# Performance work log

Measured on AMD Instinct MI355X. Metric: run time of the kernel, lower is better.

## Reference

```python
import jax, jax.numpy as jnp
import numpy as np


def _conv1d_block(x, W, b):
    # reflection pad 1 each side, conv1d k=3 stride=2, relu
    x = jnp.pad(x, ((0, 0), (0, 0), (1, 1)), mode='reflect')
    y = jax.lax.conv_general_dilated(x, W, window_strides=(2,), padding='VALID',
                                     dimension_numbers=('NCH', 'OIH', 'NCH'))
    return jax.nn.relu(y + b[None, :, None])


def setup_inputs() -> dict:
    key = jax.random.key(0)
    ks = jax.random.split(key, 8)
    C, H, E, P = 62, 256, 1024, 32768
    inp = {
        'image_x': jax.random.normal(ks[0], (C, H, H), dtype=jnp.float32),
        'corners': jax.random.uniform(ks[1], (E, 2), dtype=jnp.float32),
        'W0': jax.random.normal(ks[2], (64, C + 2, 3), dtype=jnp.float32) * 0.02,
        'b0': jnp.zeros((64,), jnp.float32),
        'W1': jax.random.normal(ks[3], (64, 64, 3), dtype=jnp.float32) * 0.02,
        'b1': jnp.zeros((64,), jnp.float32),
        'W2': jax.random.normal(ks[4], (64, 64, 3), dtype=jnp.float32) * 0.02,
        'b2': jnp.zeros((64,), jnp.float32),
        'Wf': jax.random.normal(ks[5], (64, 64), dtype=jnp.float32) * 0.05,
        'bf': jnp.zeros((64,), jnp.float32),
        'Wp': jax.random.normal(ks[6], (1, 64), dtype=jnp.float32) * 0.05,
        'bp': jnp.zeros((1,), jnp.float32),
        'num_points': P,  # static stand-in for the host-synced data-dependent count
    }
    return inp


def reference(image_x, corners, W0, b0, W1, b1, W2, b2, Wf, bf, Wp, bp, num_points):
    # edges: [E,4] = (start_xy, end_xy) with wraparound
    edges = jnp.concatenate([corners, jnp.roll(corners, -1, axis=0)], axis=-1)
    starts, ends = edges[:, :2], edges[:, 2:4]
    dirs = ends - starts                                  # [E,2]
    lengths = jnp.linalg.norm(dirs, axis=-1)              # [E]
    length_sum = lengths.sum()
    # arc-length sample offsets (num_points is static)
    offsets = jnp.arange(num_points, dtype=jnp.float32) * (length_sum / num_points)  # [P]
    el2 = jnp.cumsum(lengths)                             # [E]
    el1 = jnp.concatenate([jnp.zeros((1,), lengths.dtype), el2[:-1]])
    # per-(point, edge) interpolation parameter and bin mask
    t = (offsets[:, None] - el1[None, :]) / jnp.maximum(lengths, 1e-4)[None, :]      # [P,E]
    mask = ((offsets[:, None] >= el1[None, :]) & (offsets[:, None] < el2[None, :])).astype(jnp.float32)
    # masked reduction: sum_e mask*(start + t*dir)  (same math, no [P,E,2] temp)
    points = jnp.einsum('pe,ec->pc', mask, starts) + jnp.einsum('pe,ec->pc', mask * t, dirs)  # [P,2]
    H = image_x.shape[1]
    pr = jnp.clip(jnp.round(points * H).astype(jnp.int32), 0, H - 1)  # [P,2]
    x = image_x[:, pr[:, 0], pr[:, 1]]                    # [C,P] fancy gather
    x = jnp.concatenate([x, points.T], axis=0)[None]      # [1,C+2,P]
    x = _conv1d_block(x, W0, b0)
    x = _conv1d_block(x, W1, b1)
    x = _conv1d_block(x, W2, b2)
    x = x.max(axis=-1)                                    # [1,64]
    feat = jax.nn.relu(x @ Wf.T + bf)                     # [1,64]
    pred = jax.nn.sigmoid(feat @ Wp.T + bp).reshape(-1)   # [1]
    return feat, pred
```

## Files before the change

### kernel.cpp

```cpp
#include <hip/hip_runtime.h>
#include <hip/hip_bf16.h>
#include <math.h>

#define EDGES   32768
#define NPTS    32768
#define IMGH    256
#define L0      32768
#define L1      16384
#define L2      8192
#define L3      4096
#define S0      (L1 + 64)
#define B2      31
#define NBC     133

__global__ __launch_bounds__(512) void prep_k(const float* __restrict__ corners,
                                              const float* __restrict__ W0,
                                              const float* __restrict__ W1,
                                              const float* __restrict__ W2,
                                              const float* __restrict__ img,
                                              double* __restrict__ el2loc,
                                              double* __restrict__ partial,
                                              float*  __restrict__ Wt,
                                              float*  __restrict__ imgT)
{
    __shared__ union { double sc[512]; float tile[62][129]; } sm;
    int b = blockIdx.x, t = threadIdx.x;
    if (b < 64) {
        int e  = (b << 9) + t;
        int en = (e + 1) & (EDGES - 1);
        double dx = (double)corners[2*en]   - (double)corners[2*e];
        double dy = (double)corners[2*en+1] - (double)corners[2*e+1];
        sm.sc[t] = sqrt(dx*dx + dy*dy);
        __syncthreads();
        for (int o = 1; o < 512; o <<= 1) {
            double v = (t >= o) ? sm.sc[t - o] : 0.0;
            __syncthreads();
            sm.sc[t] += v;
            __syncthreads();
        }
        el2loc[e] = sm.sc[t];
        if (t == 511) partial[b] = sm.sc[511];
    } else if (b < 136) {
        int idx = ((b - 64) << 9) + t;
        int l   = idx / 12288;
        int rem = idx - l * 12288;
        int row = rem >> 6, o = rem & 63;
        int i   = row / 3,  k = row - i * 3;
        const float* W = (l == 0) ? W0 : ((l == 1) ? W1 : W2);
        Wt[idx] = W[o*192 + i*3 + k];
    } else {
        int pix0 = (b - 136) << 7;
        for (int idx = t; idx < 62*128; idx += 512) {
            int c = idx >> 7, p = idx & 127;
            sm.tile[c][p] = img[c * (IMGH*IMGH) + pix0 + p];
        }
        __syncthreads();
        for (int idx = t; idx < 128*64; idx += 512) {
            int p = idx >> 6, c = idx & 63;
            imgT[(size_t)(pix0 + p) * 64 + c] = (c < 62) ? sm.tile[c][p] : 0.f;
        }
    }
}

__device__ __forceinline__ void stage_ws(float ws[96][64],
                                         const float* __restrict__ Wsrc,
                                         int tid)
{
    const float4* src = (const float4*)Wsrc;
    float4 rw[6];
#pragma unroll
    for (int k = 0; k < 6; ++k) rw[k] = src[k * 256 + tid];
    float4* dst = (float4*)&ws[0][0];
#pragma unroll
    for (int k = 0; k < 6; ++k) dst[k * 256 + tid] = rw[k];
}

__device__ __forceinline__ void conv_half(float acc[16],
                                          const float xs[64][130],
                                          const float ws[96][64],
                                          int ibase, int jl2, int o0)
{
#pragma unroll 4
    for (int ii = 0; ii < 32; ++ii) {
        int i = ibase + ii;
        float x0 = xs[i][jl2], x1 = xs[i][jl2 + 1], x2 = xs[i][jl2 + 2];
        const float4* w0 = (const float4*)&ws[ii*3 + 0][o0];
        const float4* w1 = (const float4*)&ws[ii*3 + 1][o0];
        const float4* w2 = (const float4*)&ws[ii*3 + 2][o0];
#pragma unroll
        for (int q = 0; q < 4; ++q) {
            float4 a = w0[q], b = w1[q], c = w2[q];
            acc[q*4+0] = fmaf(a.x, x0, fmaf(b.x, x1, fmaf(c.x, x2, acc[q*4+0])));
            acc[q*4+1] = fmaf(a.y, x0, fmaf(b.y, x1, fmaf(c.y, x2, acc[q*4+1])));
            acc[q*4+2] = fmaf(a.z, x0, fmaf(b.z, x1, fmaf(c.z, x2, acc[q*4+2])));
            acc[q*4+3] = fmaf(a.w, x0, fmaf(b.w, x1, fmaf(c.w, x2, acc[q*4+3])));
        }
    }
}

__global__ __launch_bounds__(256) void convA_k(const float* __restrict__ corners,
                                               const double* __restrict__ el2loc,
                                               const double* __restrict__ partial,
                                               const float* __restrict__ imgT,
                                               const float* __restrict__ Wt,
                                               const float* __restrict__ bias,
                                               float* __restrict__ Y0)
{
    __shared__ float  xs[64][130];
    __shared__ float  ws[96][64];
    __shared__ double sb[64];
    int tid = threadIdx.x;
    int j0  = blockIdx.x << 6;
    int in0 = (j0 << 1) - 1;

    if (tid < 64) sb[tid] = partial[tid];
    __syncthreads();
#pragma unroll
    for (int o = 1; o < 64; o <<= 1) {
        double v = 0.0;
        if (tid < 64 && tid >= o) v = sb[tid - o];
        __syncthreads();
        if (tid < 64) sb[tid] += v;
        __syncthreads();
    }

    stage_ws(ws, Wt, tid);

    if (tid < 130) {
        int g = in0 + tid;
        if (g < 0)   g = 1;
        if (g >= L0) g = 2*L0 - 2 - g;
        double S   = sb[63];
        double off = (double)g * (S * (1.0 / (double)NPTS));
        int clo = 0, chi = 63;
        while (clo < chi) {
            int cm = (clo + chi) >> 1;
            if (sb[cm] > off) chi = cm; else clo = cm + 1;
        }
        double base = (clo == 0) ? 0.0 : sb[clo - 1];
        int lo = clo << 9, hi = lo + 511;
        while (lo < hi) {
            int mid = (lo + hi) >> 1;
            if (el2loc[mid] + base > off) hi = mid; else lo = mid + 1;
        }
        int e = lo;
        double e1 = (e == 0) ? 0.0
                  : el2loc[e-1] + (((e-1) >= 512) ? sb[((e-1) >> 9) - 1] : 0.0);
        float sxf = corners[2*e], syf = corners[2*e+1];
        int en = (e + 1) & (EDGES - 1);
        double dx = (double)corners[2*en]   - (double)sxf;
        double dy = (double)corners[2*en+1] - (double)syf;
        double len = sqrt(dx*dx + dy*dy);
        double t  = (off - e1) / fmax(len, 0.0001);
        double px = (double)sxf + t * dx;
        double py = (double)syf + t * dy;
        int r0 = (int)rint(px * (double)IMGH); r0 = r0 < 0 ? 0 : (r0 > IMGH-1 ? IMGH-1 : r0);
        int r1 = (int)rint(py * (double)IMGH); r1 = r1 < 0 ? 0 : (r1 > IMGH-1 ? IMGH-1 : r1);
        const float*  row  = imgT + (size_t)((r0 << 8) | r1) * 64;
        const float4* row4 = (const float4*)row;
        float4 rv[15];
#pragma unroll
        for (int c4 = 0; c4 < 15; ++c4) rv[c4] = row4[c4];
        float c60 = row[60], c61 = row[61];
#pragma unroll
        for (int c4 = 0; c4 < 15; ++c4) {
            xs[c4*4 + 0][tid] = rv[c4].x;
            xs[c4*4 + 1][tid] = rv[c4].y;
            xs[c4*4 + 2][tid] = rv[c4].z;
            xs[c4*4 + 3][tid] = rv[c4].w;
        }
        xs[60][tid] = c60;
        xs[61][tid] = c61;
        xs[62][tid] = (float)px;
        xs[63][tid] = (float)py;
    }
    __syncthreads();

    int lane = tid & 63;
    int o0   = (tid >> 6) << 4;
    float acc[16];
#pragma unroll
    for (int m = 0; m < 16; ++m) acc[m] = bias[o0 + m];
    int jl2 = lane << 1;

    conv_half(acc, xs, ws, 0, jl2, o0);
    __syncthreads();
    stage_ws(ws, Wt + 96*64, tid);
    __syncthreads();
    conv_half(acc, xs, ws, 32, jl2, o0);

    int j = j0 + lane;
#pragma unroll
    for (int m = 0; m < 16; ++m)
        Y0[(o0 + m) * S0 + j] = fmaxf(acc[m], 0.f);
}

__global__ __launch_bounds__(256) void convBC_k(const float* __restrict__ Y0,
                                                const float* __restrict__ Wt1,
                                                const float* __restrict__ b1,
                                                const float* __restrict__ Wt2,
                                                const float* __restrict__ b2,
                                                float* __restrict__ pmax)
{
    __shared__ float xs0[32][132];
    __shared__ float t1[64][63];
    __shared__ float ws[96][64];
    int tid = threadIdx.x;
    int b   = blockIdx.x;
    int gbase = 124*b - 3;

    int s  = tid & 63;
    int o0 = (tid >> 6) << 4;
    int j1 = 62*b - 1 + s;
    int jr = (j1 < 0) ? -j1 : (j1 > L2-1 ? L2-1 : j1);
    int col0 = 2*jr - 124*b + 2;

    {
        float r[16];
#pragma unroll
        for (int k = 0; k < 16; ++k) {
            int idx = k*256 + tid;
            int c   = idx >> 7;
            int col = idx & 127;
            int g   = gbase + col;
            if (g < 0)   g = -g;
            if (g >= L1) g = 2*L1 - 2 - g;
            r[k] = Y0[c * S0 + g];
        }
        stage_ws(ws, Wt1, tid);
#pragma unroll
        for (int k = 0; k < 16; ++k) {
            int idx = k*256 + tid;
            xs0[idx >> 7][idx & 127] = r[k];
        }
    }
    __syncthreads();

    float acc1[16];
#pragma unroll
    for (int m = 0; m < 16; ++m) acc1[m] = b1[o0 + m];

#pragma unroll 4
    for (int ii = 0; ii < 32; ++ii) {
        float x0 = xs0[ii][col0], x1 = xs0[ii][col0+1], x2 = xs0[ii][col0+2];
        const float4* w0 = (const float4*)&ws[ii*3 + 0][o0];
        const float4* w1 = (const float4*)&ws[ii*3 + 1][o0];
        const float4* w2 = (const float4*)&ws[ii*3 + 2][o0];
#pragma unroll
        for (int q = 0; q < 4; ++q) {
            float4 a = w0[q], bb = w1[q], c = w2[q];
            acc1[q*4+0] = fmaf(a.x, x0, fmaf(bb.x, x1, fmaf(c.x, x2, acc1[q*4+0])));
            acc1[q*4+1] = fmaf(a.y, x0, fmaf(bb.y, x1, fmaf(c.y, x2, acc1[q*4+1])));
            acc1[q*4+2] = fmaf(a.z, x0, fmaf(bb.z, x1, fmaf(c.z, x2, acc1[q*4+2])));
            acc1[q*4+3] = fmaf(a.w, x0, fmaf(bb.w, x1, fmaf(c.w, x2, acc1[q*4+3])));
        }
    }
    __syncthreads();

    {
        float r[16];
#pragma unroll
        for (int k = 0; k < 16; ++k) {
            int idx = k*256 + tid;
            int c   = idx >> 7;
            int col = idx & 127;
            int g   = gbase + col;
            if (g < 0)   g = -g;
            if (g >= L1) g = 2*L1 - 2 - g;
            r[k] = Y0[(32 + c) * S0 + g];
        }
        stage_ws(ws, Wt1 + 96*64, tid);
#pragma unroll
        for (int k = 0; k < 16; ++k) {
            int idx = k*256 + tid;
            xs0[idx >> 7][idx & 127] = r[k];
        }
    }
    __syncthreads();

#pragma unroll 4
    for (int ii = 0; ii < 32; ++ii) {
        float x0 = xs0[ii][col0], x1 = xs0[ii][col0+1], x2 = xs0[ii][col0+2];
        const float4* w0 = (const float4*)&ws[ii*3 + 0][o0];
        const float4* w1 = (const float4*)&ws[ii*3 + 1][o0];
        const float4* w2 = (const float4*)&ws[ii*3 + 2][o0];
#pragma unroll
        for (int q = 0; q < 4; ++q) {
            float4 a = w0[q], bb = w1[q], c = w2[q];
            acc1[q*4+0] = fmaf(a.x, x0, fmaf(bb.x, x1, fmaf(c.x, x2, acc1[q*4+0])));
            acc1[q*4+1] = fmaf(a.y, x0, fmaf(bb.y, x1, fmaf(c.y, x2, acc1[q*4+1])));
            acc1[q*4+2] = fmaf(a.z, x0, fmaf(bb.z, x1, fmaf(c.z, x2, acc1[q*4+2])));
            acc1[q*4+3] = fmaf(a.w, x0, fmaf(bb.w, x1, fmaf(c.w, x2, acc1[q*4+3])));
        }
    }
    __syncthreads();

    if (s < 63) {
#pragma unroll
        for (int m = 0; m < 16; ++m) t1[o0 + m][s] = fmaxf(acc1[m], 0.f);
    }
    __syncthreads();

    int p  = tid & 31;
    int oc = (tid >> 5) << 3;
    float acc2[8];
#pragma unroll
    for (int q = 0; q < 8; ++q) acc2[q] = b2[oc + q];

    stage_ws(ws, Wt2, tid);
    __syncthreads();
#pragma unroll 4
    for (int ii = 0; ii < 32; ++ii) {
        float x0 = t1[ii][2*p + 0], x1 = t1[ii][2*p + 1], x2 = t1[ii][2*p + 2];
        const float4* w0 = (const float4*)&ws[ii*3 + 0][oc];
        const float4* w1 = (const float4*)&ws[ii*3 + 1][oc];
        const float4* w2 = (const float4*)&ws[ii*3 + 2][oc];
#pragma unroll
        for (int q4 = 0; q4 < 2; ++q4) {
            float4 a = w0[q4], bb = w1[q4], c = w2[q4];
            acc2[q4*4+0] = fmaf(a.x, x0, fmaf(bb.x, x1, fmaf(c.x, x2, acc2[q4*4+0])));
            acc2[q4*4+1] = fmaf(a.y, x0, fmaf(bb.y, x1, fmaf(c.y, x2, acc2[q4*4+1])));
            acc2[q4*4+2] = fmaf(a.z, x0, fmaf(bb.z, x1, fmaf(c.z, x2, acc2[q4*4+2])));
            acc2[q4*4+3] = fmaf(a.w, x0, fmaf(bb.w, x1, fmaf(c.w, x2, acc2[q4*4+3])));
        }
    }
    __syncthreads();
    stage_ws(ws, Wt2 + 96*64, tid);
    __syncthreads();
#pragma unroll 4
    for (int ii = 0; ii < 32; ++ii) {
        float x0 = t1[32+ii][2*p + 0], x1 = t1[32+ii][2*p + 1], x2 = t1[32+ii][2*p + 2];
        const float4* w0 = (const float4*)&ws[ii*3 + 0][oc];
        const float4* w1 = (const float4*)&ws[ii*3 + 1][oc];
        const float4* w2 = (const float4*)&ws[ii*3 + 2][oc];
#pragma unroll
        for (int q4 = 0; q4 < 2; ++q4) {
            float4 a = w0[q4], bb = w1[q4], c = w2[q4];
            acc2[q4*4+0] = fmaf(a.x, x0, fmaf(bb.x, x1, fmaf(c.x, x2, acc2[q4*4+0])));
            acc2[q4*4+1] = fmaf(a.y, x0, fmaf(bb.y, x1, fmaf(c.y, x2, acc2[q4*4+1])));
            acc2[q4*4+2] = fmaf(a.z, x0, fmaf(bb.z, x1, fmaf(c.z, x2, acc2[q4*4+2])));
            acc2[q4*4+3] = fmaf(a.w, x0, fmaf(bb.w, x1, fmaf(c.w, x2, acc2[q4*4+3])));
        }
    }

    bool valid = (p < 31) && (31*b + p < L3);
#pragma unroll
    for (int q = 0; q < 8; ++q) {
        float v = valid ? fmaxf(acc2[q], 0.f) : 0.f;
#pragma unroll
        for (int off = 1; off < 32; off <<= 1)
            v = fmaxf(v, __shfl_xor(v, off));
        if (p == 0) pmax[b * 64 + oc + q] = v;
    }
}

__global__ __launch_bounds__(64) void fc_k(const float* __restrict__ pmax,
                                           const float* __restrict__ Wf,
                                           const float* __restrict__ bf,
                                           const float* __restrict__ Wp,
                                           const float* __restrict__ bp,
                                           float* __restrict__ out)
{
    __shared__ float cm[64];
    __shared__ float ft[64];
    int t = threadIdx.x;
    float m = 0.f;
#pragma unroll
    for (int b = 0; b < NBC; ++b) m = fmaxf(m, pmax[b * 64 + t]);
    cm[t] = m;
    __syncthreads();
    float s = bf[t];
#pragma unroll
    for (int c = 0; c < 64; ++c) s = fmaf(Wf[t*64 + c], cm[c], s);
    float f = fmaxf(s, 0.f);
    ft[t] = f;
    out[t] = f;
    __syncthreads();
    if (t == 0) {
        float z = bp[0];
#pragma unroll
        for (int c = 0; c < 64; ++c) z = fmaf(Wp[c], ft[c], z);
        out[64] = 1.f / (1.f + expf(-z));
    }
}

extern "C" void kernel_launch(void* const* d_in, const int* in_sizes, int n_in,
                              void* d_out, int out_size, void* d_ws, size_t ws_size,
                              hipStream_t stream)
{
    const float* image   = (const float*)d_in[0];
    const float* corners = (const float*)d_in[1];
    const float* W0      = (const float*)d_in[2];
    const float* b0      = (const float*)d_in[3];
    const float* W1      = (const float*)d_in[4];
    const float* b1      = (const float*)d_in[5];
    const float* W2      = (const float*)d_in[6];
    const float* b2      = (const float*)d_in[7];
    const float* Wf      = (const float*)d_in[8];
    const float* bf      = (const float*)d_in[9];
    const float* Wp      = (const float*)d_in[10];
    const float* bp      = (const float*)d_in[11];
    float* out = (float*)d_out;

    char* w = (char*)d_ws;
    double*   el2loc  = (double*)  (w);
    double*   partial = (double*)  (w + 262144);
    float*    pmax    = (float*)   (w + 262656);
    float*    Wt      = (float*)   (w + 296960);
    float*    imgT    = (float*)   (w + 444416);
    float*    Y0      = (float*)   (w + 17221632);

    prep_k   <<<648, 512, 0, stream>>>(corners, W0, W1, W2, image,
                                       el2loc, partial, Wt, imgT);
    convA_k  <<<L1 / 64, 256, 0, stream>>>(corners, el2loc, partial, imgT,
                                           Wt, b0, Y0);
    convBC_k <<<NBC, 256, 0, stream>>>(Y0, Wt + 12288, b1, Wt + 24576, b2, pmax);
    fc_k     <<<1, 64, 0, stream>>>(pmax, Wf, bf, Wp, bp, out);
}
```

Baseline: 54.72 us.

## Move point sampling into prep kernel with atomic-counter sync between blocks

Restructures the prep stage. Scan blocks shrink to 256 edges each (128 blocks) and signal completion through an atomic counter. Extra blocks in the same launch spin on that counter, then run the binary search once per point and write point coordinates and pixel indices to global memory. The image transpose now uses 64-pixel tiles with float4 loads and stores. The conv kernel no longer repeats the search (previously 130 of 256 threads per block did it, with overlap), but the change adds a memset launch and relies on the spinning blocks not starving the blocks they wait on.

```diff
diff --git a/kernel.cpp b/kernel.cpp
--- a/kernel.cpp
+++ b/kernel.cpp
@@ -10,61 +10,32 @@
 #define L2      8192
 #define L3      4096
 #define S0      (L1 + 64)
-#define B2      31
 #define NBC     133
 
-__global__ __launch_bounds__(512) void prep_k(const float* __restrict__ corners,
-                                              const float* __restrict__ W0,
-                                              const float* __restrict__ W1,
-                                              const float* __restrict__ W2,
-                                              const float* __restrict__ img,
-                                              double* __restrict__ el2loc,
-                                              double* __restrict__ partial,
-                                              float*  __restrict__ Wt,
-                                              float*  __restrict__ imgT)
-{
-    __shared__ union { double sc[512]; float tile[62][129]; } sm;
-    int b = blockIdx.x, t = threadIdx.x;
-    if (b < 64) {
-        int e  = (b << 9) + t;
-        int en = (e + 1) & (EDGES - 1);
-        double dx = (double)corners[2*en]   - (double)corners[2*e];
-        double dy = (double)corners[2*en+1] - (double)corners[2*e+1];
-        sm.sc[t] = sqrt(dx*dx + dy*dy);
-        __syncthreads();
-        for (int o = 1; o < 512; o <<= 1) {
-            double v = (t >= o) ? sm.sc[t - o] : 0.0;
-            __syncthreads();
-            sm.sc[t] += v;
-            __syncthreads();
-        }
-        el2loc[e] = sm.sc[t];
-        if (t == 511) partial[b] = sm.sc[511];
-    } else if (b < 136) {
-        int idx = ((b - 64) << 9) + t;
-        int l   = idx / 12288;
-        int rem = idx - l * 12288;
-        int row = rem >> 6, o = rem & 63;
-        int i   = row / 3,  k = row - i * 3;
-        const float* W = (l == 0) ? W0 : ((l == 1) ? W1 : W2);
-        Wt[idx] = W[o*192 + i*3 + k];
-    } else {
-        int pix0 = (b - 136) << 7;
-        for (int idx = t; idx < 62*128; idx += 512) {
-            int c = idx >> 7, p = idx & 127;
-            sm.tile[c][p] = img[c * (IMGH*IMGH) + pix0 + p];
-        }
-        __syncthreads();
-        for (int idx = t; idx < 128*64; idx += 512) {
-            int p = idx >> 6, c = idx & 63;
-            imgT[(size_t)(pix0 + p) * 64 + c] = (c < 62) ? sm.tile[c][p] : 0.f;
-        }
+#define PB_SCAN 128
+#define PB_W    18
+#define PB_T    1024
+#define PREP_GRID (PB_SCAN + PB_W + PB_T + 128)
+
+__device__ __forceinline__ void spin_until(unsigned* ctr, unsigned target, int tid)
+{
+    if (tid == 0) {
+        while (__hip_atomic_load(ctr, __ATOMIC_ACQUIRE, __HIP_MEMORY_SCOPE_AGENT) < target)
+            __builtin_amdgcn_s_sleep(2);
+    }
+    __syncthreads();
+}
+__device__ __forceinline__ void mark_done(unsigned* ctr, int tid)
+{
+    __syncthreads();
+    if (tid == 0) {
+        __threadfence();
+        __hip_atomic_fetch_add(ctr, 1u, __ATOMIC_RELEASE, __HIP_MEMORY_SCOPE_AGENT);
     }
 }
 
 __device__ __forceinline__ void stage_ws(float ws[96][64],
-                                         const float* __restrict__ Wsrc,
-                                         int tid)
+                                         const float* __restrict__ Wsrc, int tid)
 {
     const float4* src = (const float4*)Wsrc;
     float4 rw[6];
@@ -98,70 +69,150 @@
     }
 }
 
-__global__ __launch_bounds__(256) void convA_k(const float* __restrict__ corners,
-                                               const double* __restrict__ el2loc,
-                                               const double* __restrict__ partial,
-                                               const float* __restrict__ imgT,
-                                               const float* __restrict__ Wt,
-                                               const float* __restrict__ bias,
-                                               float* __restrict__ Y0)
-{
-    __shared__ float  xs[64][130];
-    __shared__ float  ws[96][64];
-    __shared__ double sb[64];
-    int tid = threadIdx.x;
-    int j0  = blockIdx.x << 6;
-    int in0 = (j0 << 1) - 1;
-
-    if (tid < 64) sb[tid] = partial[tid];
-    __syncthreads();
-#pragma unroll
-    for (int o = 1; o < 64; o <<= 1) {
-        double v = 0.0;
-        if (tid < 64 && tid >= o) v = sb[tid - o];
+__global__ __launch_bounds__(256) void prep2_k(const float* __restrict__ corners,
+                                               const float* __restrict__ W0,
+                                               const float* __restrict__ W1,
+                                               const float* __restrict__ W2,
+                                               const float* __restrict__ img,
+                                               double* __restrict__ el2loc,
+                                               double* __restrict__ partial,
+                                               float2* __restrict__ pts,
+                                               int*    __restrict__ ridx,
+                                               float*  __restrict__ Wt,
+                                               float*  __restrict__ imgT,
+                                               unsigned* __restrict__ ctr)
+{
+    __shared__ union {
+        double sc[256];
+        float  tt[64][68];
+        double sb[128];
+    } sm;
+    int b = blockIdx.x, t = threadIdx.x;
+
+    if (b < PB_SCAN) {
+        int e  = (b << 8) + t;
+        int en = (e + 1) & (EDGES - 1);
+        double dx = (double)corners[2*en]   - (double)corners[2*e];
+        double dy = (double)corners[2*en+1] - (double)corners[2*e+1];
+        sm.sc[t] = sqrt(dx*dx + dy*dy);
         __syncthreads();
-        if (tid < 64) sb[tid] += v;
+        for (int o = 1; o < 256; o <<= 1) {
+            double v = (t >= o) ? sm.sc[t - o] : 0.0;
+            __syncthreads();
+            sm.sc[t] += v;
+            __syncthreads();
+        }
+        el2loc[e] = sm.sc[t];
+        if (t == 255) partial[b] = sm.sc[255];
+        mark_done(&ctr[0], t);
+    } else if (b < PB_SCAN + PB_W) {
+        int wb = b - PB_SCAN;
+#pragma unroll
+        for (int k = 0; k < 8; ++k) {
+            int idx = wb*2048 + k*256 + t;
+            int l   = idx / 12288;
+            int rem = idx - l * 12288;
+            int row = rem >> 6, o = rem & 63;
+            int i   = row / 3,  kk = row - i * 3;
+            const float* W = (l == 0) ? W0 : ((l == 1) ? W1 : W2);
+            Wt[idx] = W[o*192 + i*3 + kk];
+        }
+    } else if (b < PB_SCAN + PB_W + PB_T) {
+        int tb   = b - (PB_SCAN + PB_W);
+        int pix0 = tb << 6;
+        const float4* img4 = (const float4*)img;
+#pragma unroll
+        for (int k = 0; k < 4; ++k) {
+            int idx = k*256 + t;
+            if (idx < 992) {
+                int c = idx >> 4, p4 = idx & 15;
+                float4 v = img4[c*16384 + (pix0 >> 2) + p4];
+                sm.tt[p4*4 + 0][c] = v.x;
+                sm.tt[p4*4 + 1][c] = v.y;
+                sm.tt[p4*4 + 2][c] = v.z;
+                sm.tt[p4*4 + 3][c] = v.w;
+            }
+        }
         __syncthreads();
-    }
-
-    stage_ws(ws, Wt, tid);
-
-    if (tid < 130) {
-        int g = in0 + tid;
-        if (g < 0)   g = 1;
-        if (g >= L0) g = 2*L0 - 2 - g;
-        double S   = sb[63];
-        double off = (double)g * (S * (1.0 / (double)NPTS));
-        int clo = 0, chi = 63;
-        while (clo < chi) {
-            int cm = (clo + chi) >> 1;
-            if (sb[cm] > off) chi = cm; else clo = cm + 1;
-        }
-        double base = (clo == 0) ? 0.0 : sb[clo - 1];
-        int lo = clo << 9, hi = lo + 511;
-        while (lo < hi) {
-            int mid = (lo + hi) >> 1;
-            if (el2loc[mid] + base > off) hi = mid; else lo = mid + 1;
-        }
+        float4* imgT4 = (float4*)imgT;
+#pragma unroll
+        for (int k = 0; k < 4; ++k) {
+            int idx = k*256 + t;
+            int p = idx >> 4, c4 = idx & 15;
+            if (c4 < 15) {
+                float4 v = *(const float4*)&sm.tt[p][c4*4];
+                imgT4[((size_t)(pix0 + p) << 4) + c4] = v;
+            } else {
+                float2 v = make_float2(sm.tt[p][60], sm.tt[p][61]);
+                *(float2*)(imgT + ((size_t)(pix0 + p) << 6) + 60) = v;
+            }
+        }
+    } else {
+        int gb = b - (PB_SCAN + PB_W + PB_T);
+        spin_until(&ctr[0], PB_SCAN, t);
+        if (t < 128) sm.sb[t] = partial[t];
+        __syncthreads();
+        for (int o = 1; o < 128; o <<= 1) {
+            double v = 0.0;
+            if (t < 128 && t >= o) v = sm.sb[t - o];
+            __syncthreads();
+            if (t < 128) sm.sb[t] += v;
+            __syncthreads();
+        }
+        int p = (gb << 8) + t;
+        double S   = sm.sb[127];
+        double off = (double)p * (S * (1.0 / (double)NPTS));
+        int clo = 0, chi = 127;
+        while (clo < chi) { int cm = (clo + chi) >> 1;
+                            if (sm.sb[cm] > off) chi = cm; else clo = cm + 1; }
+        double base = clo ? sm.sb[clo - 1] : 0.0;
+        int lo = clo << 8, hi = lo + 255;
+        while (lo < hi) { int mid = (lo + hi) >> 1;
+                          if (el2loc[mid] + base > off) hi = mid; else lo = mid + 1; }
         int e = lo;
         double e1 = (e == 0) ? 0.0
-                  : el2loc[e-1] + (((e-1) >= 512) ? sb[((e-1) >> 9) - 1] : 0.0);
+                  : el2loc[e-1] + (((e-1) >= 256) ? sm.sb[((e-1) >> 8) - 1] : 0.0);
         float sxf = corners[2*e], syf = corners[2*e+1];
         int en = (e + 1) & (EDGES - 1);
         double dx = (double)corners[2*en]   - (double)sxf;
         double dy = (double)corners[2*en+1] - (double)syf;
         double len = sqrt(dx*dx + dy*dy);
-        double t  = (off - e1) / fmax(len, 0.0001);
-        double px = (double)sxf + t * dx;
-        double py = (double)syf + t * dy;
+        double tp  = (off - e1) / fmax(len, 0.0001);
+        double px  = (double)sxf + tp * dx;
+        double py  = (double)syf + tp * dy;
         int r0 = (int)rint(px * (double)IMGH); r0 = r0 < 0 ? 0 : (r0 > IMGH-1 ? IMGH-1 : r0);
         int r1 = (int)rint(py * (double)IMGH); r1 = r1 < 0 ? 0 : (r1 > IMGH-1 ? IMGH-1 : r1);
-        const float*  row  = imgT + (size_t)((r0 << 8) | r1) * 64;
-        const float4* row4 = (const float4*)row;
+        pts[p]  = make_float2((float)px, (float)py);
+        ridx[p] = (r0 << 8) | r1;
+    }
+}
+
+__global__ __launch_bounds__(256) void convA2_k(const float2* __restrict__ pts,
+                                                const int*    __restrict__ ridx,
+                                                const float*  __restrict__ imgT,
+                                                const float*  __restrict__ Wt,
+                                                const float*  __restrict__ b0v,
+                                                float* __restrict__ Y0)
+{
+    __shared__ float xs[64][130];
+    __shared__ float ws[96][64];
+    int tid = threadIdx.x;
+    int b   = blockIdx.x;
+    int j0  = b << 6;
+    int in0 = (j0 << 1) - 1;
+
+    stage_ws(ws, Wt, tid);
+    if (tid < 130) {
+        int g = in0 + tid;
+        if (g < 0)   g = 1;
+        if (g >= L0) g = 2*L0 - 2 - g;
+        float2 pxy = pts[g];
+        int    rid = ridx[g];
+        const float4* row4 = (const float4*)(imgT + ((size_t)rid << 6));
         float4 rv[15];
 #pragma unroll
         for (int c4 = 0; c4 < 15; ++c4) rv[c4] = row4[c4];
-        float c60 = row[60], c61 = row[61];
+        float c60 = ((const float*)row4)[60], c61 = ((const float*)row4)[61];
 #pragma unroll
         for (int c4 = 0; c4 < 15; ++c4) {
             xs[c4*4 + 0][tid] = rv[c4].x;
@@ -171,8 +222,8 @@
         }
         xs[60][tid] = c60;
         xs[61][tid] = c61;
-        xs[62][tid] = (float)px;
-        xs[63][tid] = (float)py;
+        xs[62][tid] = pxy.x;
+        xs[63][tid] = pxy.y;
     }
     __syncthreads();
 
@@ -180,7 +231,7 @@
     int o0   = (tid >> 6) << 4;
     float acc[16];
 #pragma unroll
-    for (int m = 0; m < 16; ++m) acc[m] = bias[o0 + m];
+    for (int m = 0; m < 16; ++m) acc[m] = b0v[o0 + m];
     int jl2 = lane << 1;
 
     conv_half(acc, xs, ws, 0, jl2, o0);
@@ -220,8 +271,7 @@
 #pragma unroll
         for (int k = 0; k < 16; ++k) {
             int idx = k*256 + tid;
-            int c   = idx >> 7;
-            int col = idx & 127;
+            int c   = idx >> 7, col = idx & 127;
             int g   = gbase + col;
             if (g < 0)   g = -g;
             if (g >= L1) g = 2*L1 - 2 - g;
@@ -239,7 +289,6 @@
     float acc1[16];
 #pragma unroll
     for (int m = 0; m < 16; ++m) acc1[m] = b1[o0 + m];
-
 #pragma unroll 4
     for (int ii = 0; ii < 32; ++ii) {
         float x0 = xs0[ii][col0], x1 = xs0[ii][col0+1], x2 = xs0[ii][col0+2];
@@ -256,14 +305,12 @@
         }
     }
     __syncthreads();
-
     {
         float r[16];
 #pragma unroll
         for (int k = 0; k < 16; ++k) {
             int idx = k*256 + tid;
-            int c   = idx >> 7;
-            int col = idx & 127;
+            int c   = idx >> 7, col = idx & 127;
             int g   = gbase + col;
             if (g < 0)   g = -g;
             if (g >= L1) g = 2*L1 - 2 - g;
@@ -277,7 +324,6 @@
         }
     }
     __syncthreads();
-
 #pragma unroll 4
     for (int ii = 0; ii < 32; ++ii) {
         float x0 = xs0[ii][col0], x1 = xs0[ii][col0+1], x2 = xs0[ii][col0+2];
@@ -294,7 +340,6 @@
         }
     }
     __syncthreads();
-
     if (s < 63) {
 #pragma unroll
         for (int m = 0; m < 16; ++m) t1[o0 + m][s] = fmaxf(acc1[m], 0.f);
@@ -403,17 +448,20 @@
     float* out = (float*)d_out;
 
     char* w = (char*)d_ws;
-    double*   el2loc  = (double*)  (w);
-    double*   partial = (double*)  (w + 262144);
-    float*    pmax    = (float*)   (w + 262656);
-    float*    Wt      = (float*)   (w + 296960);
-    float*    imgT    = (float*)   (w + 444416);
-    float*    Y0      = (float*)   (w + 17221632);
-
-    prep_k   <<<648, 512, 0, stream>>>(corners, W0, W1, W2, image,
-                                       el2loc, partial, Wt, imgT);
-    convA_k  <<<L1 / 64, 256, 0, stream>>>(corners, el2loc, partial, imgT,
-                                           Wt, b0, Y0);
+    unsigned* ctr     = (unsigned*)(w);
+    double*   el2loc  = (double*)  (w + 256);
+    double*   partial = (double*)  (w + 262400);
+    float2*   pts     = (float2*)  (w + 263424);
+    int*      ridx    = (int*)     (w + 525568);
+    float*    pmax    = (float*)   (w + 656640);
+    float*    Wt      = (float*)   (w + 690688);
+    float*    imgT    = (float*)   (w + 838144);
+    float*    Y0      = (float*)   (w + 17615360);
+
+    hipMemsetAsync(ctr, 0, 256, stream);
+    prep2_k  <<<PREP_GRID, 256, 0, stream>>>(corners, W0, W1, W2, image,
+                                             el2loc, partial, pts, ridx, Wt, imgT, ctr);
+    convA2_k <<<256, 256, 0, stream>>>(pts, ridx, imgT, Wt, b0, Y0);
     convBC_k <<<NBC, 256, 0, stream>>>(Y0, Wt + 12288, b1, Wt + 24576, b2, pmax);
     fc_k     <<<1, 64, 0, stream>>>(pmax, Wf, bf, Wp, bp, out);
 }
```

After: 74.85 us. 36.8% more time.
